# Optimization experiments

Hardware: AMD Instinct MI355X
Metric: run time of the kernel (lower is better)

## Reference

```python
import jax, jax.numpy as jnp
import numpy as np

N_LIT, N_CLAUSE, N_EDGES, D = 100000, 400000, 1200000, 128


def setup_inputs() -> dict:
    key = jax.random.key(0)
    ks = jax.random.split(key, 9)
    s = 1.0 / np.sqrt(D)  # PyTorch LSTM init: U(-1/sqrt(hidden), 1/sqrt(hidden))
    x_l = jax.random.normal(ks[0], (N_LIT, D), jnp.float32)
    h0 = jax.random.normal(ks[1], (N_CLAUSE, D), jnp.float32)
    c0 = jax.random.normal(ks[2], (N_CLAUSE, D), jnp.float32)
    W_ih = jax.random.uniform(ks[3], (4 * D, D), jnp.float32, -s, s)
    W_hh = jax.random.uniform(ks[4], (4 * D, D), jnp.float32, -s, s)
    b_ih = jax.random.uniform(ks[5], (4 * D,), jnp.float32, -s, s)
    b_hh = jax.random.uniform(ks[6], (4 * D,), jnp.float32, -s, s)
    edge_lit = jax.random.randint(ks[7], (N_EDGES,), 0, N_LIT, jnp.int32)
    edge_clause = jnp.sort(jax.random.randint(ks[8], (N_EDGES,), 0, N_CLAUSE, jnp.int32))
    return {"x_l": x_l, "h0": h0, "c0": c0, "W_ih": W_ih, "W_hh": W_hh,
            "b_ih": b_ih, "b_hh": b_hh, "edge_lit": edge_lit, "edge_clause": edge_clause}


def reference(x_l, h0, c0, W_ih, W_hh, b_ih, b_hh, edge_lit, edge_clause):
    n_clauses = h0.shape[0]
    # msg = adj_t @ x_l : sparse aggregation of literal features into clauses
    msg = jax.ops.segment_sum(x_l[edge_lit], edge_clause, num_segments=n_clauses)  # [n_clauses, D]
    # Single-timestep LSTM cell (seq_len=1, batch=n_clauses); PyTorch gate order i,f,g,o
    gates = msg @ W_ih.T + b_ih + h0 @ W_hh.T + b_hh  # [n_clauses, 4D]
    i, f, g, o = jnp.split(gates, 4, axis=-1)
    i = jax.nn.sigmoid(i)
    f = jax.nn.sigmoid(f)
    g = jnp.tanh(g)
    o = jax.nn.sigmoid(o)
    c_new = f * c0 + i * g
    h_new = o * jnp.tanh(c_new)
    return (h_new, c_new)
```

## Files before the change

kernel.cpp:

```cpp
#include <hip/hip_runtime.h>
#include <hip/hip_bf16.h>


using frag_ab = __attribute__((ext_vector_type(8))) short;
using frag_cd = __attribute__((ext_vector_type(4))) float;

__device__ __forceinline__ float bf2f(unsigned short u) {
    union { unsigned u; float f; } v; v.u = ((unsigned)u) << 16; return v.f;
}
__device__ __forceinline__ unsigned short f2bf(float f) {
    __hip_bfloat16 h = __float2bfloat16(f);
    return *reinterpret_cast<unsigned short*>(&h);
}
__device__ __forceinline__ float sigm(float x) {
    return __builtin_amdgcn_rcpf(1.0f + __builtin_amdgcn_exp2f(-1.442695040889f * x));
}
__device__ __forceinline__ float tanh_fast(float x) {
    float s = __builtin_amdgcn_rcpf(1.0f + __builtin_amdgcn_exp2f(-2.885390081777f * x));
    return __builtin_fmaf(2.0f, s, -1.0f);
}
__device__ __forceinline__ frag_ab load8_fp32(const float* p) {
    float4 a = *reinterpret_cast<const float4*>(p);
    float4 b = *reinterpret_cast<const float4*>(p + 4);
    frag_ab r;
    r[0] = (short)f2bf(a.x); r[1] = (short)f2bf(a.y);
    r[2] = (short)f2bf(a.z); r[3] = (short)f2bf(a.w);
    r[4] = (short)f2bf(b.x); r[5] = (short)f2bf(b.y);
    r[6] = (short)f2bf(b.z); r[7] = (short)f2bf(b.w);
    return r;
}

#define WS_BPACK_OFF  0
#define WS_BIAS_OFF   262144
#define WS_FLAG_OFF   264192
#define WS_ROWPTR_OFF 264704

#define EDGE_CAP 512

__global__ void detect_fmt(const unsigned short* __restrict__ x, int* __restrict__ flag) {
    int t = threadIdx.x;
    int cnt = 0;
    for (int i = t; i < 4096; i += 64) {
        unsigned e = (x[2 * i] >> 7) & 0xFF;
        cnt += (e >= 0xC0) ? 1 : 0;
    }
    #pragma unroll
    for (int s = 32; s; s >>= 1) cnt += __shfl_xor(cnt, s);
    if (t == 0) *flag = (cnt > 64) ? 1 : 0;
}

__global__ void build_rowptr(const int* __restrict__ edge_clause, int* __restrict__ rowptr,
                             int n_edges, int n_clause) {
    int idx = blockIdx.x * blockDim.x + threadIdx.x;
    if (idx > n_clause) return;
    int lo = 0, hi = n_edges;
    while (lo < hi) {
        int mid = (lo + hi) >> 1;
        if (edge_clause[mid] < idx) lo = mid + 1; else hi = mid;
    }
    rowptr[idx] = lo;
}

template <int FP32IN>
__global__ void prepack(const void* __restrict__ W_ih_, const void* __restrict__ W_hh_,
                        const void* __restrict__ b_ih_, const void* __restrict__ b_hh_,
                        unsigned short* __restrict__ Bpack, float* __restrict__ bias,
                        const int* __restrict__ flag) {
    if (*flag != FP32IN) return;
    int idx = blockIdx.x * blockDim.x + threadIdx.x;
    if (idx < 16384) {
        int kk = idx >> 11;
        int n  = (idx >> 2) & 511;
        int lq = idx & 3;
        int ksrc = (kk & 3) * 32 + lq * 8;
        frag_ab v;
        if constexpr (FP32IN) {
            const float* W = (kk < 4) ? (const float*)W_ih_ : (const float*)W_hh_;
            v = load8_fp32(W + (size_t)n * 128 + ksrc);
        } else {
            const unsigned short* W =
                (kk < 4) ? (const unsigned short*)W_ih_ : (const unsigned short*)W_hh_;
            v = *reinterpret_cast<const frag_ab*>(W + (size_t)n * 128 + ksrc);
        }
        *reinterpret_cast<frag_ab*>(Bpack + (size_t)idx * 8) = v;
    }
    if (idx < 512) {
        float b;
        if constexpr (FP32IN)
            b = ((const float*)b_ih_)[idx] + ((const float*)b_hh_)[idx];
        else
            b = bf2f(((const unsigned short*)b_ih_)[idx]) +
                bf2f(((const unsigned short*)b_hh_)[idx]);
        bias[idx] = b;
    }
}

template <int FP32IN>
__global__ __launch_bounds__(512, 4) void lit2clause_fused(
    const void* __restrict__ x_l_,
    const void* __restrict__ h0_,
    const void* __restrict__ c0_,
    const unsigned short* __restrict__ Bpack,
    const float* __restrict__ bias,
    const int*  __restrict__ rowptr_g,
    const int*  __restrict__ edge_lit,
    void* __restrict__ out_,
    const int* __restrict__ fmt_flag,
    int n_clause)
{
    if (*fmt_flag != FP32IN) return;

    __shared__ __align__(16) unsigned char SH[32768];
    __shared__ int elits[EDGE_CAP];
    unsigned char* Amsg = SH;
    unsigned char* Ah0  = SH + 16384;
    float* LDSf = (float*)SH;

    const int tid  = threadIdx.x;
    const int lane = tid & 63;
    const int w    = tid >> 6;
    const int cbase = blockIdx.x * 64;

    int rp_l = 0;
    if (lane < 9) rp_l = rowptr_g[cbase + w * 8 + lane];

    const int eBase = rowptr_g[cbase];
    const int eEnd  = rowptr_g[cbase + 64];
    const int eCount = eEnd - eBase;
    for (int i = tid; i < eCount && i < EDGE_CAP; i += 512)
        elits[i] = edge_lit[eBase + i];

    #pragma unroll
    for (int q0 = 0; q0 < 2; ++q0) {
        int q = tid + q0 * 512;
        int row = q >> 4;
        int j   = q & 15;
        frag_ab v;
        if constexpr (FP32IN) {
            v = load8_fp32((const float*)h0_ + (size_t)(cbase + row) * 128 + j * 8);
        } else {
            v = *reinterpret_cast<const frag_ab*>(
                (const unsigned short*)h0_ + (size_t)(cbase + row) * 128 + j * 8);
        }
        int byte = (j * 16) ^ ((row & 7) << 4);
        *reinterpret_cast<frag_ab*>(Ah0 + row * 256 + byte) = v;
    }
    __syncthreads();

    {
        const int q   = lane >> 4;
        const int l16 = lane & 15;
        for (int s = 0; s < 8; ++s) {
            int cc = w * 8 + s;
            int st = __shfl(rp_l, s)     - eBase;
            int en = __shfl(rp_l, s + 1) - eBase;
            float a[8] = {0.f, 0.f, 0.f, 0.f, 0.f, 0.f, 0.f, 0.f};
            for (int e = st + q; e < en; e += 4) {
                int lit = (e < EDGE_CAP) ? elits[e] : edge_lit[eBase + e];
                if constexpr (FP32IN) {
                    const float* xr = (const float*)x_l_ + (size_t)lit * 128 + l16 * 8;
                    float4 v0 = *reinterpret_cast<const float4*>(xr);
                    float4 v1 = *reinterpret_cast<const float4*>(xr + 4);
                    a[0] += v0.x; a[1] += v0.y; a[2] += v0.z; a[3] += v0.w;
                    a[4] += v1.x; a[5] += v1.y; a[6] += v1.z; a[7] += v1.w;
                } else {
                    const unsigned short* xr =
                        (const unsigned short*)x_l_ + (size_t)lit * 128 + l16 * 8;
                    frag_ab v = *reinterpret_cast<const frag_ab*>(xr);
                    #pragma unroll
                    for (int j = 0; j < 8; ++j) a[j] += bf2f((unsigned short)v[j]);
                }
            }
            #pragma unroll
            for (int j = 0; j < 8; ++j) {
                a[j] += __shfl_xor(a[j], 16);
                a[j] += __shfl_xor(a[j], 32);
            }
            if (q == 0) {
                frag_ab o;
                #pragma unroll
                for (int j = 0; j < 8; ++j) o[j] = (short)f2bf(a[j]);
                int byte = (l16 * 16) ^ ((cc & 7) << 4);
                *reinterpret_cast<frag_ab*>(Amsg + cc * 256 + byte) = o;
            }
        }
    }
    __syncthreads();

    const int l15 = lane & 15;
    const int lq  = lane >> 4;
    const int d = w * 16 + l15;

    float cold[4][4];
    #pragma unroll
    for (int mf = 0; mf < 4; ++mf) {
        #pragma unroll
        for (int r = 0; r < 4; ++r) {
            int m = cbase + mf * 16 + lq * 4 + r;
            if constexpr (FP32IN) cold[mf][r] = ((const float*)c0_)[(size_t)m * 128 + d];
            else cold[mf][r] = bf2f(((const unsigned short*)c0_)[(size_t)m * 128 + d]);
        }
    }

    frag_cd acc[4][4];
    #pragma unroll
    for (int g = 0; g < 4; ++g)
        #pragma unroll
        for (int mf = 0; mf < 4; ++mf)
            acc[g][mf] = (frag_cd){0.f, 0.f, 0.f, 0.f};

    const frag_ab* Bp = reinterpret_cast<const frag_ab*>(Bpack);
    float bi[4];
    #pragma unroll
    for (int g = 0; g < 4; ++g) bi[g] = bias[g * 128 + d];

    #pragma unroll
    for (int kk = 0; kk < 8; ++kk) {
        const unsigned char* At = (kk < 4) ? Amsg : Ah0;
        frag_ab afr[4];
        #pragma unroll
        for (int mf = 0; mf < 4; ++mf) {
            int row = mf * 16 + l15;
            int byte = ((kk & 3) * 64 + lq * 16) ^ ((row & 7) << 4);
            afr[mf] = *reinterpret_cast<const frag_ab*>(At + row * 256 + byte);
        }
        frag_ab bfr[4];
        #pragma unroll
        for (int g = 0; g < 4; ++g) {
            int n = g * 128 + w * 16 + l15;
            bfr[g] = Bp[(kk * 512 + n) * 4 + lq];
        }
        #pragma unroll
        for (int g = 0; g < 4; ++g)
            #pragma unroll
            for (int mf = 0; mf < 4; ++mf)
                acc[g][mf] = __builtin_amdgcn_mfma_f32_16x16x32_bf16(
                    afr[mf], bfr[g], acc[g][mf], 0, 0, 0);
    }

    #pragma unroll
    for (int mf = 0; mf < 4; ++mf) {
        #pragma unroll
        for (int r = 0; r < 4; ++r) {
            float gi = acc[0][mf][r] + bi[0];
            float gf = acc[1][mf][r] + bi[1];
            float gg = acc[2][mf][r] + bi[2];
            float go = acc[3][mf][r] + bi[3];
            float iv = sigm(gi);
            float fv = sigm(gf);
            float gv = tanh_fast(gg);
            float ov = sigm(go);
            float cn = fv * cold[mf][r] + iv * gv;
            float hn = ov * tanh_fast(cn);
            acc[0][mf][r] = hn;
            acc[1][mf][r] = cn;
        }
    }

    #pragma unroll
    for (int half = 0; half < 2; ++half) {
        __syncthreads();
        #pragma unroll
        for (int mf = 0; mf < 4; ++mf) {
            #pragma unroll
            for (int r = 0; r < 4; ++r) {
                int rl = mf * 16 + lq * 4 + r;
                int idx = rl * 128 + ((((d >> 2) ^ (rl & 7)) << 2) | (d & 3));
                LDSf[idx] = acc[half][mf][r];
            }
        }
        __syncthreads();
        if constexpr (FP32IN) {
            float* outp = (float*)out_ + (size_t)half * n_clause * 128;
            #pragma unroll
            for (int q0 = 0; q0 < 4; ++q0) {
                int q = tid + q0 * 512;
                int row = q >> 5;
                int j   = q & 31;
                float4 v = *reinterpret_cast<const float4*>(
                    &LDSf[row * 128 + ((j ^ (row & 7)) << 2)]);
                *reinterpret_cast<float4*>(outp + (size_t)(cbase + row) * 128 + j * 4) = v;
            }
        } else {
            unsigned short* outp = (unsigned short*)out_ + (size_t)half * n_clause * 128;
            #pragma unroll
            for (int q0 = 0; q0 < 2; ++q0) {
                int q = tid + q0 * 512;
                int row = q >> 4;
                int jj  = q & 15;
                int j0 = 2 * jj, j1 = 2 * jj + 1;
                float4 f0 = *reinterpret_cast<const float4*>(
                    &LDSf[row * 128 + ((j0 ^ (row & 7)) << 2)]);
                float4 f1 = *reinterpret_cast<const float4*>(
                    &LDSf[row * 128 + ((j1 ^ (row & 7)) << 2)]);
                frag_ab o;
                o[0] = (short)f2bf(f0.x); o[1] = (short)f2bf(f0.y);
                o[2] = (short)f2bf(f0.z); o[3] = (short)f2bf(f0.w);
                o[4] = (short)f2bf(f1.x); o[5] = (short)f2bf(f1.y);
                o[6] = (short)f2bf(f1.z); o[7] = (short)f2bf(f1.w);
                *reinterpret_cast<frag_ab*>(outp + (size_t)(cbase + row) * 128 + jj * 8) = o;
            }
        }
    }
}

extern "C" void kernel_launch(void* const* d_in, const int* in_sizes, int n_in,
                              void* d_out, int out_size, void* d_ws, size_t ws_size,
                              hipStream_t stream) {
    const void* x_l  = d_in[0];
    const void* h0   = d_in[1];
    const void* c0   = d_in[2];
    const void* W_ih = d_in[3];
    const void* W_hh = d_in[4];
    const void* b_ih = d_in[5];
    const void* b_hh = d_in[6];
    const int* edge_lit    = (const int*)d_in[7];
    const int* edge_clause = (const int*)d_in[8];

    int n_edges  = in_sizes[7];
    int n_clause = in_sizes[1] / 128;
    int nblocks  = (n_clause + 63) / 64;

    unsigned char* ws = (unsigned char*)d_ws;
    unsigned short* Bpack = (unsigned short*)(ws + WS_BPACK_OFF);
    float* bias  = (float*)(ws + WS_BIAS_OFF);
    int* flag    = (int*)(ws + WS_FLAG_OFF);
    int* rowptr  = (int*)(ws + WS_ROWPTR_OFF);

    detect_fmt<<<1, 64, 0, stream>>>((const unsigned short*)x_l, flag);

    build_rowptr<<<(n_clause + 256) / 256, 256, 0, stream>>>(
        edge_clause, rowptr, n_edges, n_clause);

    prepack<1><<<64, 256, 0, stream>>>(W_ih, W_hh, b_ih, b_hh, Bpack, bias, flag);
    prepack<0><<<64, 256, 0, stream>>>(W_ih, W_hh, b_ih, b_hh, Bpack, bias, flag);

    lit2clause_fused<1><<<nblocks, 512, 0, stream>>>(
        x_l, h0, c0, Bpack, bias, rowptr, edge_lit, d_out, flag, n_clause);
    lit2clause_fused<0><<<nblocks, 512, 0, stream>>>(
        x_l, h0, c0, Bpack, bias, rowptr, edge_lit, d_out, flag, n_clause);
}
```

Before: 346.2 us.

## Balance edge gather across threads with LDS fp32 atomic accumulation

```diff
diff --git a/kernel.cpp b/kernel.cpp
--- a/kernel.cpp
+++ b/kernel.cpp
@@ -36,6 +36,12 @@
 #define WS_ROWPTR_OFF 264704
 
 #define EDGE_CAP 512
+#define MROW 132
+
+#define SH_BYTES 54272
+#define OFF_AH0  33792
+#define OFF_ELIT 50176
+#define OFF_ECLA 52224
 
 __global__ void detect_fmt(const unsigned short* __restrict__ x, int* __restrict__ flag) {
     int t = threadIdx.x;
@@ -104,16 +110,19 @@
     const float* __restrict__ bias,
     const int*  __restrict__ rowptr_g,
     const int*  __restrict__ edge_lit,
+    const int*  __restrict__ edge_clause,
     void* __restrict__ out_,
     const int* __restrict__ fmt_flag,
     int n_clause)
 {
     if (*fmt_flag != FP32IN) return;
 
-    __shared__ __align__(16) unsigned char SH[32768];
-    __shared__ int elits[EDGE_CAP];
+    __shared__ __align__(16) unsigned char SH[SH_BYTES];
+    float* msgF32 = (float*)SH;
     unsigned char* Amsg = SH;
-    unsigned char* Ah0  = SH + 16384;
+    unsigned char* Ah0  = SH + OFF_AH0;
+    int* elits = (int*)(SH + OFF_ELIT);
+    int* eclau = (int*)(SH + OFF_ECLA);
     float* LDSf = (float*)SH;
 
     const int tid  = threadIdx.x;
@@ -121,14 +130,17 @@
     const int w    = tid >> 6;
     const int cbase = blockIdx.x * 64;
 
-    int rp_l = 0;
-    if (lane < 9) rp_l = rowptr_g[cbase + w * 8 + lane];
-
     const int eBase = rowptr_g[cbase];
     const int eEnd  = rowptr_g[cbase + 64];
     const int eCount = eEnd - eBase;
-    for (int i = tid; i < eCount && i < EDGE_CAP; i += 512)
+
+    for (int q = tid; q < (64 * MROW) / 4; q += 512)
+        *reinterpret_cast<float4*>(msgF32 + q * 4) = (float4){0.f, 0.f, 0.f, 0.f};
+
+    for (int i = tid; i < eCount && i < EDGE_CAP; i += 512) {
         elits[i] = edge_lit[eBase + i];
+        eclau[i] = edge_clause[eBase + i];
+    }
 
     #pragma unroll
     for (int q0 = 0; q0 < 2; ++q0) {
@@ -148,42 +160,61 @@
     __syncthreads();
 
     {
-        const int q   = lane >> 4;
-        const int l16 = lane & 15;
-        for (int s = 0; s < 8; ++s) {
-            int cc = w * 8 + s;
-            int st = __shfl(rp_l, s)     - eBase;
-            int en = __shfl(rp_l, s + 1) - eBase;
-            float a[8] = {0.f, 0.f, 0.f, 0.f, 0.f, 0.f, 0.f, 0.f};
-            for (int e = st + q; e < en; e += 4) {
-                int lit = (e < EDGE_CAP) ? elits[e] : edge_lit[eBase + e];
-                if constexpr (FP32IN) {
-                    const float* xr = (const float*)x_l_ + (size_t)lit * 128 + l16 * 8;
-                    float4 v0 = *reinterpret_cast<const float4*>(xr);
-                    float4 v1 = *reinterpret_cast<const float4*>(xr + 4);
-                    a[0] += v0.x; a[1] += v0.y; a[2] += v0.z; a[3] += v0.w;
-                    a[4] += v1.x; a[5] += v1.y; a[6] += v1.z; a[7] += v1.w;
-                } else {
-                    const unsigned short* xr =
-                        (const unsigned short*)x_l_ + (size_t)lit * 128 + l16 * 8;
-                    frag_ab v = *reinterpret_cast<const frag_ab*>(xr);
-                    #pragma unroll
-                    for (int j = 0; j < 8; ++j) a[j] += bf2f((unsigned short)v[j]);
-                }
+        const int g   = tid >> 4;
+        const int l16 = tid & 15;
+        const int len = (eCount + 31) >> 5;
+        const int gStart = g * len;
+        for (int i = 0; i < len; ++i) {
+            int e = gStart + i;
+            if (e >= eCount) break;
+            int lit, cl;
+            if (e < EDGE_CAP) { lit = elits[e]; cl = eclau[e]; }
+            else { lit = edge_lit[eBase + e]; cl = edge_clause[eBase + e]; }
+            int row = cl - cbase;
+            float* dst = msgF32 + row * MROW + l16 * 8;
+            if constexpr (FP32IN) {
+                const float* xr = (const float*)x_l_ + (size_t)lit * 128 + l16 * 8;
+                float4 v0 = *reinterpret_cast<const float4*>(xr);
+                float4 v1 = *reinterpret_cast<const float4*>(xr + 4);
+                atomicAdd(dst + 0, v0.x); atomicAdd(dst + 1, v0.y);
+                atomicAdd(dst + 2, v0.z); atomicAdd(dst + 3, v0.w);
+                atomicAdd(dst + 4, v1.x); atomicAdd(dst + 5, v1.y);
+                atomicAdd(dst + 6, v1.z); atomicAdd(dst + 7, v1.w);
+            } else {
+                const unsigned short* xr =
+                    (const unsigned short*)x_l_ + (size_t)lit * 128 + l16 * 8;
+                frag_ab v = *reinterpret_cast<const frag_ab*>(xr);
+                #pragma unroll
+                for (int j = 0; j < 8; ++j)
+                    atomicAdd(dst + j, bf2f((unsigned short)v[j]));
             }
-            #pragma unroll
-            for (int j = 0; j < 8; ++j) {
-                a[j] += __shfl_xor(a[j], 16);
-                a[j] += __shfl_xor(a[j], 32);
-            }
-            if (q == 0) {
-                frag_ab o;
-                #pragma unroll
-                for (int j = 0; j < 8; ++j) o[j] = (short)f2bf(a[j]);
-                int byte = (l16 * 16) ^ ((cc & 7) << 4);
-                *reinterpret_cast<frag_ab*>(Amsg + cc * 256 + byte) = o;
-            }
-        }
+        }
+    }
+    __syncthreads();
+
+    float4 rc[2][2];
+    #pragma unroll
+    for (int q0 = 0; q0 < 2; ++q0) {
+        int q = tid + q0 * 512;
+        int row = q >> 4;
+        int jj  = q & 15;
+        const float* src = msgF32 + row * MROW + jj * 8;
+        rc[q0][0] = *reinterpret_cast<const float4*>(src);
+        rc[q0][1] = *reinterpret_cast<const float4*>(src + 4);
+    }
+    __syncthreads();
+    #pragma unroll
+    for (int q0 = 0; q0 < 2; ++q0) {
+        int q = tid + q0 * 512;
+        int row = q >> 4;
+        int jj  = q & 15;
+        frag_ab o;
+        o[0] = (short)f2bf(rc[q0][0].x); o[1] = (short)f2bf(rc[q0][0].y);
+        o[2] = (short)f2bf(rc[q0][0].z); o[3] = (short)f2bf(rc[q0][0].w);
+        o[4] = (short)f2bf(rc[q0][1].x); o[5] = (short)f2bf(rc[q0][1].y);
+        o[6] = (short)f2bf(rc[q0][1].z); o[7] = (short)f2bf(rc[q0][1].w);
+        int byte = (jj * 16) ^ ((row & 7) << 4);
+        *reinterpret_cast<frag_ab*>(Amsg + row * 256 + byte) = o;
     }
     __syncthreads();
 
@@ -336,7 +367,7 @@
     prepack<0><<<64, 256, 0, stream>>>(W_ih, W_hh, b_ih, b_hh, Bpack, bias, flag);
 
     lit2clause_fused<1><<<nblocks, 512, 0, stream>>>(
-        x_l, h0, c0, Bpack, bias, rowptr, edge_lit, d_out, flag, n_clause);
+        x_l, h0, c0, Bpack, bias, rowptr, edge_lit, edge_clause, d_out, flag, n_clause);
     lit2clause_fused<0><<<nblocks, 512, 0, stream>>>(
-        x_l, h0, c0, Bpack, bias, rowptr, edge_lit, d_out, flag, n_clause);
-}
+        x_l, h0, c0, Bpack, bias, rowptr, edge_lit, edge_clause, d_out, flag, n_clause);
+}
```

Result: slower. 904.3 us (+161.2%).

## Split fused gather+LSTM kernel into separate gather and GEMM kernels

Applied to the files above, without the earlier changes.

```diff
diff --git a/kernel.cpp b/kernel.cpp
--- a/kernel.cpp
+++ b/kernel.cpp
@@ -96,12 +96,8 @@
 }
 
 template <int FP32IN>
-__global__ __launch_bounds__(512, 4) void lit2clause_fused(
+__global__ __launch_bounds__(512, 8) void gather_msg(
     const void* __restrict__ x_l_,
-    const void* __restrict__ h0_,
-    const void* __restrict__ c0_,
-    const unsigned short* __restrict__ Bpack,
-    const float* __restrict__ bias,
     const int*  __restrict__ rowptr_g,
     const int*  __restrict__ edge_lit,
     void* __restrict__ out_,
@@ -110,26 +106,100 @@
 {
     if (*fmt_flag != FP32IN) return;
 
-    __shared__ __align__(16) unsigned char SH[32768];
     __shared__ int elits[EDGE_CAP];
-    unsigned char* Amsg = SH;
-    unsigned char* Ah0  = SH + 16384;
-    float* LDSf = (float*)SH;
-
     const int tid  = threadIdx.x;
     const int lane = tid & 63;
     const int w    = tid >> 6;
     const int cbase = blockIdx.x * 64;
 
+    unsigned short* msgb;
+    if constexpr (FP32IN) msgb = (unsigned short*)((float*)out_ + (size_t)n_clause * 128);
+    else                  msgb = (unsigned short*)out_ + (size_t)n_clause * 128;
+    constexpr int MSTRIDE = FP32IN ? 256 : 128;
+
     int rp_l = 0;
     if (lane < 9) rp_l = rowptr_g[cbase + w * 8 + lane];
-
     const int eBase = rowptr_g[cbase];
     const int eEnd  = rowptr_g[cbase + 64];
     const int eCount = eEnd - eBase;
     for (int i = tid; i < eCount && i < EDGE_CAP; i += 512)
         elits[i] = edge_lit[eBase + i];
-
+    __syncthreads();
+
+    const int q   = lane >> 4;
+    const int l16 = lane & 15;
+    for (int s = 0; s < 8; ++s) {
+        int st = __shfl(rp_l, s)     - eBase;
+        int en = __shfl(rp_l, s + 1) - eBase;
+        float a[8] = {0.f, 0.f, 0.f, 0.f, 0.f, 0.f, 0.f, 0.f};
+        for (int e = st + q; e < en; e += 4) {
+            int lit = (e < EDGE_CAP) ? elits[e] : edge_lit[eBase + e];
+            if constexpr (FP32IN) {
+                const float* xr = (const float*)x_l_ + (size_t)lit * 128 + l16 * 8;
+                float4 v0 = *reinterpret_cast<const float4*>(xr);
+                float4 v1 = *reinterpret_cast<const float4*>(xr + 4);
+                a[0] += v0.x; a[1] += v0.y; a[2] += v0.z; a[3] += v0.w;
+                a[4] += v1.x; a[5] += v1.y; a[6] += v1.z; a[7] += v1.w;
+            } else {
+                const unsigned short* xr =
+                    (const unsigned short*)x_l_ + (size_t)lit * 128 + l16 * 8;
+                frag_ab v = *reinterpret_cast<const frag_ab*>(xr);
+                #pragma unroll
+                for (int j = 0; j < 8; ++j) a[j] += bf2f((unsigned short)v[j]);
+            }
+        }
+        #pragma unroll
+        for (int j = 0; j < 8; ++j) {
+            a[j] += __shfl_xor(a[j], 16);
+            a[j] += __shfl_xor(a[j], 32);
+        }
+        if (q == 0) {
+            frag_ab o;
+            #pragma unroll
+            for (int j = 0; j < 8; ++j) o[j] = (short)f2bf(a[j]);
+            *reinterpret_cast<frag_ab*>(
+                msgb + (size_t)(cbase + w * 8 + s) * MSTRIDE + l16 * 8) = o;
+        }
+    }
+}
+
+template <int FP32IN>
+__global__ __launch_bounds__(512, 4) void gemm_lstm(
+    const void* __restrict__ h0_,
+    const void* __restrict__ c0_,
+    const unsigned short* __restrict__ Bpack,
+    const float* __restrict__ bias,
+    void* __restrict__ out_,
+    const int* __restrict__ fmt_flag,
+    int n_clause)
+{
+    if (*fmt_flag != FP32IN) return;
+
+    __shared__ __align__(16) unsigned char SH[32768];
+    unsigned char* Amsg = SH;
+    unsigned char* Ah0  = SH + 16384;
+    float* LDSf = (float*)SH;
+
+    const int tid  = threadIdx.x;
+    const int lane = tid & 63;
+    const int w    = tid >> 6;
+    const int cbase = blockIdx.x * 64;
+
+    unsigned short* msgb;
+    if constexpr (FP32IN) msgb = (unsigned short*)((float*)out_ + (size_t)n_clause * 128);
+    else                  msgb = (unsigned short*)out_ + (size_t)n_clause * 128;
+    constexpr int MSTRIDE = FP32IN ? 256 : 128;
+
+    #pragma unroll
+    for (int q0 = 0; q0 < 2; ++q0) {
+        int q = tid + q0 * 512;
+        int row = q >> 4;
+        int j   = q & 15;
+        frag_ab v = *reinterpret_cast<const frag_ab*>(
+            msgb + (size_t)(cbase + row) * MSTRIDE + j * 8);
+        int byte = (j * 16) ^ ((row & 7) << 4);
+        *reinterpret_cast<frag_ab*>(Amsg + row * 256 + byte) = v;
+    }
     #pragma unroll
     for (int q0 = 0; q0 < 2; ++q0) {
         int q = tid + q0 * 512;
@@ -144,46 +214,6 @@
         }
         int byte = (j * 16) ^ ((row & 7) << 4);
         *reinterpret_cast<frag_ab*>(Ah0 + row * 256 + byte) = v;
-    }
-    __syncthreads();
-
-    {
-        const int q   = lane >> 4;
-        const int l16 = lane & 15;
-        for (int s = 0; s < 8; ++s) {
-            int cc = w * 8 + s;
-            int st = __shfl(rp_l, s)     - eBase;
-            int en = __shfl(rp_l, s + 1) - eBase;
-            float a[8] = {0.f, 0.f, 0.f, 0.f, 0.f, 0.f, 0.f, 0.f};
-            for (int e = st + q; e < en; e += 4) {
-                int lit = (e < EDGE_CAP) ? elits[e] : edge_lit[eBase + e];
-                if constexpr (FP32IN) {
-                    const float* xr = (const float*)x_l_ + (size_t)lit * 128 + l16 * 8;
-                    float4 v0 = *reinterpret_cast<const float4*>(xr);
-                    float4 v1 = *reinterpret_cast<const float4*>(xr + 4);
-                    a[0] += v0.x; a[1] += v0.y; a[2] += v0.z; a[3] += v0.w;
-                    a[4] += v1.x; a[5] += v1.y; a[6] += v1.z; a[7] += v1.w;
-                } else {
-                    const unsigned short* xr =
-                        (const unsigned short*)x_l_ + (size_t)lit * 128 + l16 * 8;
-                    frag_ab v = *reinterpret_cast<const frag_ab*>(xr);
-                    #pragma unroll
-                    for (int j = 0; j < 8; ++j) a[j] += bf2f((unsigned short)v[j]);
-                }
-            }
-            #pragma unroll
-            for (int j = 0; j < 8; ++j) {
-                a[j] += __shfl_xor(a[j], 16);
-                a[j] += __shfl_xor(a[j], 32);
-            }
-            if (q == 0) {
-                frag_ab o;
-                #pragma unroll
-                for (int j = 0; j < 8; ++j) o[j] = (short)f2bf(a[j]);
-                int byte = (l16 * 16) ^ ((cc & 7) << 4);
-                *reinterpret_cast<frag_ab*>(Amsg + cc * 256 + byte) = o;
-            }
-        }
     }
     __syncthreads();
 
@@ -335,8 +365,13 @@
     prepack<1><<<64, 256, 0, stream>>>(W_ih, W_hh, b_ih, b_hh, Bpack, bias, flag);
     prepack<0><<<64, 256, 0, stream>>>(W_ih, W_hh, b_ih, b_hh, Bpack, bias, flag);
 
-    lit2clause_fused<1><<<nblocks, 512, 0, stream>>>(
-        x_l, h0, c0, Bpack, bias, rowptr, edge_lit, d_out, flag, n_clause);
-    lit2clause_fused<0><<<nblocks, 512, 0, stream>>>(
-        x_l, h0, c0, Bpack, bias, rowptr, edge_lit, d_out, flag, n_clause);
-}
+    gather_msg<1><<<nblocks, 512, 0, stream>>>(
+        x_l, rowptr, edge_lit, d_out, flag, n_clause);
+    gather_msg<0><<<nblocks, 512, 0, stream>>>(
+        x_l, rowptr, edge_lit, d_out, flag, n_clause);
+
+    gemm_lstm<1><<<nblocks, 512, 0, stream>>>(
+        h0, c0, Bpack, bias, d_out, flag, n_clause);
+    gemm_lstm<0><<<nblocks, 512, 0, stream>>>(
+        h0, c0, Bpack, bias, d_out, flag, n_clause);
+}
```

Result: slower. 367.4 us (+6.1%).

## Shrink fused LSTM block to 32 clauses with 4 waves each covering 32 columns

Applied to the files above, without the earlier changes.

```diff
diff --git a/kernel.cpp b/kernel.cpp
--- a/kernel.cpp
+++ b/kernel.cpp
@@ -35,7 +35,7 @@
 #define WS_FLAG_OFF   264192
 #define WS_ROWPTR_OFF 264704
 
-#define EDGE_CAP 512
+#define EDGE_CAP 256
 
 __global__ void detect_fmt(const unsigned short* __restrict__ x, int* __restrict__ flag) {
     int t = threadIdx.x;
@@ -96,7 +96,7 @@
 }
 
 template <int FP32IN>
-__global__ __launch_bounds__(512, 4) void lit2clause_fused(
+__global__ __launch_bounds__(256, 4) void lit2clause_fused(
     const void* __restrict__ x_l_,
     const void* __restrict__ h0_,
     const void* __restrict__ c0_,
@@ -110,29 +110,29 @@
 {
     if (*fmt_flag != FP32IN) return;
 
-    __shared__ __align__(16) unsigned char SH[32768];
+    __shared__ __align__(16) unsigned char SH[16384];
     __shared__ int elits[EDGE_CAP];
     unsigned char* Amsg = SH;
-    unsigned char* Ah0  = SH + 16384;
+    unsigned char* Ah0  = SH + 8192;
     float* LDSf = (float*)SH;
 
     const int tid  = threadIdx.x;
     const int lane = tid & 63;
     const int w    = tid >> 6;
-    const int cbase = blockIdx.x * 64;
+    const int cbase = blockIdx.x * 32;
 
     int rp_l = 0;
     if (lane < 9) rp_l = rowptr_g[cbase + w * 8 + lane];
 
     const int eBase = rowptr_g[cbase];
-    const int eEnd  = rowptr_g[cbase + 64];
+    const int eEnd  = rowptr_g[cbase + 32];
     const int eCount = eEnd - eBase;
-    for (int i = tid; i < eCount && i < EDGE_CAP; i += 512)
+    for (int i = tid; i < eCount && i < EDGE_CAP; i += 256)
         elits[i] = edge_lit[eBase + i];
 
     #pragma unroll
     for (int q0 = 0; q0 < 2; ++q0) {
-        int q = tid + q0 * 512;
+        int q = tid + q0 * 256;
         int row = q >> 4;
         int j   = q & 15;
         frag_ab v;
@@ -189,71 +189,86 @@
 
     const int l15 = lane & 15;
     const int lq  = lane >> 4;
-    const int d = w * 16 + l15;
-
-    float cold[4][4];
-    #pragma unroll
-    for (int mf = 0; mf < 4; ++mf) {
-        #pragma unroll
-        for (int r = 0; r < 4; ++r) {
-            int m = cbase + mf * 16 + lq * 4 + r;
-            if constexpr (FP32IN) cold[mf][r] = ((const float*)c0_)[(size_t)m * 128 + d];
-            else cold[mf][r] = bf2f(((const unsigned short*)c0_)[(size_t)m * 128 + d]);
-        }
-    }
-
-    frag_cd acc[4][4];
+
+    float cold[2][2][4];
+    #pragma unroll
+    for (int nf = 0; nf < 2; ++nf) {
+        int d = w * 32 + nf * 16 + l15;
+        #pragma unroll
+        for (int mf = 0; mf < 2; ++mf) {
+            #pragma unroll
+            for (int r = 0; r < 4; ++r) {
+                int m = cbase + mf * 16 + lq * 4 + r;
+                if constexpr (FP32IN)
+                    cold[nf][mf][r] = ((const float*)c0_)[(size_t)m * 128 + d];
+                else
+                    cold[nf][mf][r] = bf2f(((const unsigned short*)c0_)[(size_t)m * 128 + d]);
+            }
+        }
+    }
+
+    frag_cd acc[4][2][2];
     #pragma unroll
     for (int g = 0; g < 4; ++g)
         #pragma unroll
-        for (int mf = 0; mf < 4; ++mf)
-            acc[g][mf] = (frag_cd){0.f, 0.f, 0.f, 0.f};
+        for (int nf = 0; nf < 2; ++nf)
+            #pragma unroll
+            for (int mf = 0; mf < 2; ++mf)
+                acc[g][nf][mf] = (frag_cd){0.f, 0.f, 0.f, 0.f};
 
     const frag_ab* Bp = reinterpret_cast<const frag_ab*>(Bpack);
-    float bi[4];
-    #pragma unroll
-    for (int g = 0; g < 4; ++g) bi[g] = bias[g * 128 + d];
 
     #pragma unroll
     for (int kk = 0; kk < 8; ++kk) {
         const unsigned char* At = (kk < 4) ? Amsg : Ah0;
-        frag_ab afr[4];
-        #pragma unroll
-        for (int mf = 0; mf < 4; ++mf) {
+        frag_ab afr[2];
+        #pragma unroll
+        for (int mf = 0; mf < 2; ++mf) {
             int row = mf * 16 + l15;
             int byte = ((kk & 3) * 64 + lq * 16) ^ ((row & 7) << 4);
             afr[mf] = *reinterpret_cast<const frag_ab*>(At + row * 256 + byte);
         }
-        frag_ab bfr[4];
         #pragma unroll
         for (int g = 0; g < 4; ++g) {
-            int n = g * 128 + w * 16 + l15;
-            bfr[g] = Bp[(kk * 512 + n) * 4 + lq];
-        }
-        #pragma unroll
-        for (int g = 0; g < 4; ++g)
-            #pragma unroll
-            for (int mf = 0; mf < 4; ++mf)
-                acc[g][mf] = __builtin_amdgcn_mfma_f32_16x16x32_bf16(
-                    afr[mf], bfr[g], acc[g][mf], 0, 0, 0);
-    }
-
-    #pragma unroll
-    for (int mf = 0; mf < 4; ++mf) {
-        #pragma unroll
-        for (int r = 0; r < 4; ++r) {
-            float gi = acc[0][mf][r] + bi[0];
-            float gf = acc[1][mf][r] + bi[1];
-            float gg = acc[2][mf][r] + bi[2];
-            float go = acc[3][mf][r] + bi[3];
-            float iv = sigm(gi);
-            float fv = sigm(gf);
-            float gv = tanh_fast(gg);
-            float ov = sigm(go);
-            float cn = fv * cold[mf][r] + iv * gv;
-            float hn = ov * tanh_fast(cn);
-            acc[0][mf][r] = hn;
-            acc[1][mf][r] = cn;
+            frag_ab bfr[2];
+            #pragma unroll
+            for (int nf = 0; nf < 2; ++nf) {
+                int n = g * 128 + w * 32 + nf * 16 + l15;
+                bfr[nf] = Bp[(kk * 512 + n) * 4 + lq];
+            }
+            #pragma unroll
+            for (int nf = 0; nf < 2; ++nf)
+                #pragma unroll
+                for (int mf = 0; mf < 2; ++mf)
+                    acc[g][nf][mf] = __builtin_amdgcn_mfma_f32_16x16x32_bf16(
+                        afr[mf], bfr[nf], acc[g][nf][mf], 0, 0, 0);
+        }
+    }
+
+    #pragma unroll
+    for (int nf = 0; nf < 2; ++nf) {
+        int d = w * 32 + nf * 16 + l15;
+        float bi0 = bias[0 * 128 + d];
+        float bi1 = bias[1 * 128 + d];
+        float bi2 = bias[2 * 128 + d];
+        float bi3 = bias[3 * 128 + d];
+        #pragma unroll
+        for (int mf = 0; mf < 2; ++mf) {
+            #pragma unroll
+            for (int r = 0; r < 4; ++r) {
+                float gi = acc[0][nf][mf][r] + bi0;
+                float gf = acc[1][nf][mf][r] + bi1;
+                float gg = acc[2][nf][mf][r] + bi2;
+                float go = acc[3][nf][mf][r] + bi3;
+                float iv = sigm(gi);
+                float fv = sigm(gf);
+                float gv = tanh_fast(gg);
+                float ov = sigm(go);
+                float cn = fv * cold[nf][mf][r] + iv * gv;
+                float hn = ov * tanh_fast(cn);
+                acc[0][nf][mf][r] = hn;
+                acc[1][nf][mf][r] = cn;
+            }
         }
     }
 
@@ -261,12 +276,16 @@
     for (int half = 0; half < 2; ++half) {
         __syncthreads();
         #pragma unroll
-        for (int mf = 0; mf < 4; ++mf) {
-            #pragma unroll
-            for (int r = 0; r < 4; ++r) {
-                int rl = mf * 16 + lq * 4 + r;
-                int idx = rl * 128 + ((((d >> 2) ^ (rl & 7)) << 2) | (d & 3));
-                LDSf[idx] = acc[half][mf][r];
+        for (int nf = 0; nf < 2; ++nf) {
+            int d = w * 32 + nf * 16 + l15;
+            #pragma unroll
+            for (int mf = 0; mf < 2; ++mf) {
+                #pragma unroll
+                for (int r = 0; r < 4; ++r) {
+                    int rl = mf * 16 + lq * 4 + r;
+                    int idx = rl * 128 + ((((d >> 2) ^ (rl & 7)) << 2) | (d & 3));
+                    LDSf[idx] = acc[half][nf][mf][r];
+                }
             }
         }
         __syncthreads();
@@ -274,7 +293,7 @@
             float* outp = (float*)out_ + (size_t)half * n_clause * 128;
             #pragma unroll
             for (int q0 = 0; q0 < 4; ++q0) {
-                int q = tid + q0 * 512;
+                int q = tid + q0 * 256;
                 int row = q >> 5;
                 int j   = q & 31;
                 float4 v = *reinterpret_cast<const float4*>(
@@ -285,7 +304,7 @@
             unsigned short* outp = (unsigned short*)out_ + (size_t)half * n_clause * 128;
             #pragma unroll
             for (int q0 = 0; q0 < 2; ++q0) {
-                int q = tid + q0 * 512;
+                int q = tid + q0 * 256;
                 int row = q >> 4;
                 int jj  = q & 15;
                 int j0 = 2 * jj, j1 = 2 * jj + 1;
@@ -319,7 +338,7 @@
 
     int n_edges  = in_sizes[7];
     int n_clause = in_sizes[1] / 128;
-    int nblocks  = (n_clause + 63) / 64;
+    int nblocks  = (n_clause + 31) / 32;
 
     unsigned char* ws = (unsigned char*)d_ws;
     unsigned short* Bpack = (unsigned short*)(ws + WS_BPACK_OFF);
@@ -335,8 +354,8 @@
     prepack<1><<<64, 256, 0, stream>>>(W_ih, W_hh, b_ih, b_hh, Bpack, bias, flag);
     prepack<0><<<64, 256, 0, stream>>>(W_ih, W_hh, b_ih, b_hh, Bpack, bias, flag);
 
-    lit2clause_fused<1><<<nblocks, 512, 0, stream>>>(
+    lit2clause_fused<1><<<nblocks, 256, 0, stream>>>(
         x_l, h0, c0, Bpack, bias, rowptr, edge_lit, d_out, flag, n_clause);
-    lit2clause_fused<0><<<nblocks, 512, 0, stream>>>(
+    lit2clause_fused<0><<<nblocks, 256, 0, stream>>>(
         x_l, h0, c0, Bpack, bias, rowptr, edge_lit, d_out, flag, n_clause);
 }
```

Result: slower. 440.7 us (+27.3%).
